# Performance work log

Hardware: AMD Instinct MI355X
Metric: run time of the kernel (lower is better)

The kernel has to match this reference:

```python
import jax, jax.numpy as jnp
from jax import lax
import numpy as np

EPS = 1e-5


def _conv3x3(x, W, stride):
    # x: [N,C,H,W], W: [O,I,3,3]
    return lax.conv_general_dilated(
        x, W, window_strides=(stride, stride), padding=((1, 1), (1, 1)),
        dimension_numbers=("NCHW", "OIHW", "NCHW"))


def _bn(x, gamma, beta):
    # training-mode BatchNorm2d: batch statistics over (N,H,W)
    mean = jnp.mean(x, axis=(0, 2, 3), keepdims=True)
    var = jnp.var(x, axis=(0, 2, 3), keepdims=True)
    inv = lax.rsqrt(var + EPS)
    return (x - mean) * inv * gamma[None, :, None, None] + beta[None, :, None, None]


def setup_inputs() -> dict:
    key = jax.random.key(0)
    ks = jax.random.split(key, 5)
    N, C, H, W = 32, 256, 56, 56
    x = jax.random.normal(ks[0], (N, C, H, W), dtype=jnp.float32)
    W1 = jax.random.normal(ks[1], (C, C, 3, 3), dtype=jnp.float32) * 0.05
    W2 = jax.random.normal(ks[2], (C, C, 3, 3), dtype=jnp.float32) * 0.05
    gamma1 = jnp.ones((C,), jnp.float32)
    beta1 = jnp.zeros((C,), jnp.float32)
    gamma2 = jnp.ones((C,), jnp.float32)
    beta2 = jnp.zeros((C,), jnp.float32)
    mask1 = jax.random.randint(ks[3], (C,), 0, 2).astype(jnp.float32)
    mask2 = jax.random.randint(ks[4], (C,), 0, 2).astype(jnp.float32)
    return {"x": x, "W1": W1, "W2": W2, "gamma1": gamma1, "beta1": beta1,
            "gamma2": gamma2, "beta2": beta2, "mask1": mask1, "mask2": mask2}


def reference(x, W1, W2, gamma1, beta1, gamma2, beta2, mask1, mask2):
    # conv_with_mask: output channels with mask==0 stay zero (structured pruning)
    h = _conv3x3(x, W1, 1) * mask1[None, :, None, None]
    h = jax.nn.relu(_bn(h, gamma1, beta1))
    h = _conv3x3(h, W2, 1) * mask2[None, :, None, None]
    h = _bn(h, gamma2, beta2)
    # stride=1, in_planes==planes -> identity shortcut
    return jax.nn.relu(h + x)
```

## Files before the change

kernel.cpp:

```cpp
#include <hip/hip_runtime.h>

#define N_   32
#define C_   256
#define H_   56
#define W_   56
#define HW_  (H_ * W_)
#define NHW_ (N_ * HW_)
#define PLANE_ ((size_t)NHW_ * 32)

typedef unsigned short u16;
typedef __attribute__((ext_vector_type(8))) short short8;
typedef __attribute__((ext_vector_type(4))) float f32x4;

__device__ __forceinline__ float b2f(u16 u) {
    union { unsigned int i; float f; } v; v.i = ((unsigned int)u) << 16; return v.f;
}
__device__ __forceinline__ u16 f2b(float f) {
    union { float f; unsigned int i; } v; v.f = f;
    unsigned int r = v.i + 0x7fffu + ((v.i >> 16) & 1u);
    return (u16)(r >> 16);
}

typedef const __attribute__((address_space(1))) unsigned int* as1_u32p;
typedef __attribute__((address_space(3))) unsigned int* as3_u32p;
__device__ __forceinline__ void gload_lds16(const u16* g, u16* l) {
    __builtin_amdgcn_global_load_lds((as1_u32p)g, (as3_u32p)l, 16, 0, 0);
}

extern "C" __global__ __launch_bounds__(256) void cvt_x_kernel(
    const float* __restrict__ x, u16* __restrict__ xb)
{
    __shared__ float t[64 * 57];
    const int nh = blockIdx.x, n = nh / H_, h = nh % H_;
    const size_t pix0 = (size_t)(n * H_ + h) * W_;
    for (int cb = 0; cb < 4; ++cb) {
        __syncthreads();
        for (int idx = threadIdx.x; idx < 64 * 56; idx += 256) {
            int cc = idx / 56, w = idx % 56;
            t[cc * 57 + w] = x[(((size_t)(n * C_ + cb * 64 + cc)) * H_ + h) * W_ + w];
        }
        __syncthreads();
        for (int idx = threadIdx.x; idx < 56 * 64; idx += 256) {
            int w = idx >> 6, cc = idx & 63;
            int plane = cb * 2 + (cc >> 5);
            xb[(size_t)plane * PLANE_ + (pix0 + w) * 32 + (cc & 31)] = f2b(t[cc * 57 + w]);
        }
    }
}

extern "C" __global__ void mask_scan_kernel(
    const float* __restrict__ m1, const float* __restrict__ m2,
    int* __restrict__ p1, int* __restrict__ p2,
    float* __restrict__ mp1, float* __restrict__ mp2,
    int* __restrict__ k1, int* __restrict__ k2, int* __restrict__ id256)
{
    const float* mask  = blockIdx.x ? m2 : m1;
    int*   perm  = blockIdx.x ? p2 : p1;
    float* maskp = blockIdx.x ? mp2 : mp1;
    int*   kpar  = blockIdx.x ? k2 : k1;
    __shared__ float m[256];
    const int c = threadIdx.x;
    m[c] = mask[c];
    if (blockIdx.x == 0) id256[c] = c;
    __syncthreads();
    int pre = 0, tot = 0;
    for (int i = 0; i < 256; ++i) {
        int nz = (m[i] != 0.f) ? 1 : 0;
        if (i < c) pre += nz;
        tot += nz;
    }
    const int nz = (m[c] != 0.f) ? 1 : 0;
    const int pos = nz ? pre : tot + (c - pre);
    perm[pos] = c;
    maskp[pos] = m[c];
    if (c == 0) {
        kpar[0] = ((tot + 15) >> 4) << 4;
        kpar[1] = 8;
        kpar[2] = tot;
        kpar[3] = 0;
    }
    if (c < 8) kpar[4 + c] = c;
}

extern "C" __global__ void chunk_sel_kernel(
    const float* __restrict__ shift, const int* __restrict__ kparK,
    int* __restrict__ kpar)
{
    __shared__ int act[8];
    const int c = threadIdx.x;
    if (c < 8) act[c] = 0;
    __syncthreads();
    const int K = kparK[2];
    const bool a = (c < K) || (shift[c] > 0.f);
    if (a) atomicOr(&act[c >> 5], 1);
    __syncthreads();
    if (c == 0) {
        int nq = 0;
        for (int q = 0; q < 8; ++q) if (act[q]) kpar[4 + nq++] = q;
        kpar[1] = nq;
    }
}

extern "C" __global__ __launch_bounds__(256) void pack_w_kernel(
    const float* __restrict__ w, const int* __restrict__ operm,
    const int* __restrict__ iperm, u16* __restrict__ wp)
{
    int o = blockIdx.x * 256 + threadIdx.x;
    int j = o & 7, lq = (o >> 3) & 3, l15 = (o >> 5) & 15;
    int cog = (o >> 9) & 15, cih = (o >> 13) & 7, rs = o >> 16;
    int co = operm[cog * 16 + l15];
    int ci = iperm[cih * 32 + lq * 8 + j];
    wp[o] = f2b(w[((size_t)co * C_ + ci) * 9 + rs]);
}

extern "C" __global__ __launch_bounds__(256, 3) void BasicBlock_4355096838467_kernel(
    const u16* __restrict__ xb,
    const u16* __restrict__ wpA,
    const float* __restrict__ maskp,
    const u16* __restrict__ zeropad,
    const int* __restrict__ kp,
    u16* __restrict__ outb)
{
    __shared__ u16 lds[3][7680];

    const int tid  = threadIdx.x;
    const int wave = tid >> 6, lane = tid & 63;
    const int l15  = lane & 15, lq = lane >> 4;
    const int wave_co = wave >> 1, wave_px = wave & 1;
    const int xcd = blockIdx.x & 7, r_ = blockIdx.x >> 3;
    const int yco = r_ & 1;

    const int Kc = kp[0];
    if (Kc <= yco * 128) return;
    const int nq = kp[1];

    const int sb  = xcd * 112 + (r_ >> 1);
    const int n = sb / 28, hb = sb % 28;
    const int h0 = hb * 2;
    const int cog_base = yco * 8 + wave_co * 4;
    const size_t abase0 = (size_t)cog_base * 512 + (size_t)(l15 * 32 + lq * 8);

    int nf = (Kc >> 4) - cog_base;
    nf = nf < 0 ? 0 : (nf > 4 ? 4 : nf);

    f32x4 acc[4][4];
#pragma unroll
    for (int i = 0; i < 4; ++i)
#pragma unroll
        for (int j = 0; j < 4; ++j) acc[i][j] = (f32x4){0.f, 0.f, 0.f, 0.f};

    auto stage = [&](int q, int b) {
        const u16* plane = xb + (size_t)q * PLANE_;
        for (int is = wave; is < 15; is += 4) {
            int L = is * 64 + lane;
            int pixel = L >> 2, so = L & 3;
            int rr = pixel / 58, slot = pixel - rr * 58;
            int oct = so ^ ((slot >> 1) & 3);
            int row = h0 - 1 + rr, col = slot - 1;
            bool ok = pixel < 232 &&
                      (unsigned)row < (unsigned)H_ && (unsigned)col < (unsigned)W_;
            const u16* gp = ok
                ? plane + ((size_t)(n * H_ + row) * W_ + col) * 32 + oct * 8
                : zeropad + oct * 8;
            gload_lds16(gp, &lds[b][is * 512]);
        }
    };

    short8 afq[3][4];
    auto loadA = [&](int rs_, int q, short8 dst[4]) {
        const size_t bb = (size_t)rs_ * 65536 + (size_t)q * 8192 + abase0;
#pragma unroll
        for (int fm = 0; fm < 4; ++fm)
            if (fm < nf) dst[fm] = *(const short8*)(wpA + bb + (size_t)fm * 512);
    };

    if (nq > 0) {
        const int q0 = kp[4];
        stage(q0, 0);
        __builtin_amdgcn_sched_barrier(0);
        loadA(0, q0, afq[0]);
        loadA(1, q0, afq[1]);
        __builtin_amdgcn_sched_barrier(0);
        if (nq > 1) {
            stage(kp[5], 1);
            __builtin_amdgcn_sched_barrier(0);
            asm volatile("s_waitcnt vmcnt(3)" ::: "memory");
        } else {
            asm volatile("s_waitcnt vmcnt(0)" ::: "memory");
        }
        __builtin_amdgcn_sched_barrier(0);
        __builtin_amdgcn_s_barrier();
        __builtin_amdgcn_sched_barrier(0);

        for (int t = 0; t < nq; ++t) {
            const int q  = kp[4 + t];
            const int qn = kp[4 + (t + 1 < nq ? t + 1 : t)];
            const u16* Lb = &lds[t % 3][0];
            if (nf > 0) {
#pragma unroll
                for (int rs = 0; rs < 9; ++rs) {
                    if (rs < 7) loadA(rs + 2, q, afq[(rs + 2) % 3]);
                    else        loadA(rs - 7, qn, afq[(rs + 2) % 3]);
                    const int r = rs / 3, s = rs - (rs / 3) * 3;
                    short8 bf[4];
#pragma unroll
                    for (int fn = 0; fn < 4; ++fn) {
                        int slot = fn * 16 + l15 + s;
                        int pixel = (wave_px + r) * 58 + slot;
                        int so = lq ^ ((slot >> 1) & 3);
                        bf[fn] = *(const short8*)(Lb + pixel * 32 + so * 8);
                    }
                    __builtin_amdgcn_s_setprio(1);
#pragma unroll
                    for (int fm = 0; fm < 4; ++fm)
                        if (fm < nf) {
#pragma unroll
                            for (int fn = 0; fn < 4; ++fn)
                                acc[fm][fn] = __builtin_amdgcn_mfma_f32_16x16x32_bf16(
                                    afq[rs % 3][fm], bf[fn], acc[fm][fn], 0, 0, 0);
                        }
                    __builtin_amdgcn_s_setprio(0);
                }
            }
            __builtin_amdgcn_sched_barrier(0);
            if (t + 2 < nq) stage(kp[6 + t], (t + 2) % 3);
            __builtin_amdgcn_sched_barrier(0);
            if (t + 1 < nq) {
                if (t + 2 < nq) asm volatile("s_waitcnt vmcnt(3)" ::: "memory");
                else            asm volatile("s_waitcnt vmcnt(0)" ::: "memory");
                __builtin_amdgcn_sched_barrier(0);
                __builtin_amdgcn_s_barrier();
                __builtin_amdgcn_sched_barrier(0);
            }
        }
    }

    const int row = h0 + wave_px;
#pragma unroll
    for (int fn = 0; fn < 4; ++fn) {
        int px = fn * 16 + l15;
        if (px < W_) {
#pragma unroll
            for (int fm = 0; fm < 4; ++fm) {
                int co_b = cog_base * 16 + fm * 16 + lq * 4;
                const f32x4 mk = *(const f32x4*)(maskp + co_b);
                size_t base = (size_t)(co_b >> 5) * PLANE_
                            + ((size_t)(n * H_ + row) * W_ + px) * 32 + (co_b & 31);
                ushort4 o;
                o.x = f2b(acc[fm][fn][0] * mk[0]);
                o.y = f2b(acc[fm][fn][1] * mk[1]);
                o.z = f2b(acc[fm][fn][2] * mk[2]);
                o.w = f2b(acc[fm][fn][3] * mk[3]);
                *(ushort4*)(outb + base) = o;
            }
        }
    }
}

extern "C" __global__ void zero_accum_kernel(float* __restrict__ p) {
    p[blockIdx.x * 256 + threadIdx.x] = 0.f;
}

extern "C" __global__ __launch_bounds__(256) void stats_nhwc_kernel(
    const u16* __restrict__ hb, const int* __restrict__ kp,
    float* __restrict__ gsum, float* __restrict__ gsq)
{
    __shared__ float s_s[8 * 256];
    __shared__ float s_q[8 * 256];
    const int g = threadIdx.x >> 5, l = threadIdx.x & 31;
    const size_t pbase_off = (size_t)(l >> 2) * PLANE_ + (l & 3) * 8;
    const bool live = kp[2] > 128 * (l >> 4);
    float s[8], q[8];
#pragma unroll
    for (int j = 0; j < 8; ++j) { s[j] = 0.f; q[j] = 0.f; }
    const int pbase = blockIdx.x * 256;
    if (live) {
        for (int t = 0; t < 32; ++t) {
            int p = pbase + g + t * 8;
            short8 v = *(const short8*)(hb + pbase_off + (size_t)p * 32);
#pragma unroll
            for (int j = 0; j < 8; ++j) {
                float f = b2f((u16)v[j]);
                s[j] += f; q[j] += f * f;
            }
        }
    }
#pragma unroll
    for (int j = 0; j < 8; ++j) {
        s_s[g * 256 + l * 8 + j] = s[j];
        s_q[g * 256 + l * 8 + j] = q[j];
    }
    __syncthreads();
    const int c = threadIdx.x;
    float S = 0.f, Q = 0.f;
#pragma unroll
    for (int g2 = 0; g2 < 8; ++g2) { S += s_s[g2 * 256 + c]; Q += s_q[g2 * 256 + c]; }
    atomicAdd(&gsum[c], S);
    atomicAdd(&gsq[c], Q);
}

extern "C" __global__ void finalize_bn_kernel(
    const float* __restrict__ gsum, const float* __restrict__ gsq,
    const float* __restrict__ gamma, const float* __restrict__ beta,
    const int* __restrict__ perm,
    float* __restrict__ scale, float* __restrict__ shift)
{
    const int c = threadIdx.x;
    const int co = perm[c];
    const float inv_n = 1.f / (float)NHW_;
    float mean = gsum[c] * inv_n;
    float var  = gsq[c] * inv_n - mean * mean;
    var = fmaxf(var, 0.f);
    float inv = rsqrtf(var + 1e-5f);
    float sc = gamma[co] * inv;
    scale[c] = sc;
    shift[c] = beta[co] - mean * sc;
}

extern "C" __global__ __launch_bounds__(256) void bn_relu_nhwc_kernel(
    u16* __restrict__ hb, const float* __restrict__ scale,
    const float* __restrict__ shift, const int* __restrict__ kp)
{
    size_t idx = ((size_t)blockIdx.x * 256 + threadIdx.x) * 8;
    const int plane = (int)(blockIdx.x / 1568);
    const int c0 = plane * 32 + (int)(idx & 31);
    short8 o;
    if (kp[2] > 128 * (plane >> 2)) {
        short8 v = *(short8*)(hb + idx);
#pragma unroll
        for (int j = 0; j < 8; ++j) {
            float f = b2f((u16)v[j]) * scale[c0 + j] + shift[c0 + j];
            o[j] = (short)f2b(fmaxf(f, 0.f));
        }
    } else {
#pragma unroll
        for (int j = 0; j < 8; ++j)
            o[j] = (short)f2b(fmaxf(shift[c0 + j], 0.f));
    }
    *(short8*)(hb + idx) = o;
}

extern "C" __global__ __launch_bounds__(256) void bn_add_relu_out_kernel(
    const u16* __restrict__ h2b, const float* __restrict__ x,
    const float* __restrict__ scale, const float* __restrict__ shift,
    const int* __restrict__ perm, const int* __restrict__ kp,
    float* __restrict__ out)
{
    __shared__ float t[64 * 57];
    const int nh = blockIdx.x, n = nh / H_, h = nh % H_;
    const size_t pix0 = (size_t)(n * H_ + h) * W_;
    const int K2 = kp[2];
    for (int cb = 0; cb < 4; ++cb) {
        __syncthreads();
        for (int it = threadIdx.x; it < 448; it += 256) {
            int w = it >> 3, oc = it & 7;
            int plane = cb * 2 + (oc >> 2);
            short8 v = {0, 0, 0, 0, 0, 0, 0, 0};
            if (K2 > 128 * (plane >> 2)) {
                size_t addr = (size_t)plane * PLANE_ + (pix0 + w) * 32 + (oc & 3) * 8;
                v = *(const short8*)(h2b + addr);
            }
#pragma unroll
            for (int j = 0; j < 8; ++j) t[(oc * 8 + j) * 57 + w] = b2f((u16)v[j]);
        }
        __syncthreads();
        for (int it = threadIdx.x; it < 64 * 56; it += 256) {
            int cl = it / 56, w = it % 56;
            int c = cb * 64 + cl;
            int co = perm[c];
            size_t oidx = ((size_t)(n * C_ + co) * H_ + h) * W_ + w;
            float v = t[cl * 57 + w] * scale[c] + shift[c] + x[oidx];
            out[oidx] = fmaxf(v, 0.f);
        }
    }
}

extern "C" void kernel_launch(void* const* d_in, const int* in_sizes, int n_in,
                              void* d_out, int out_size, void* d_ws, size_t ws_size,
                              hipStream_t stream) {
    const float* x      = (const float*)d_in[0];
    const float* W1     = (const float*)d_in[1];
    const float* W2     = (const float*)d_in[2];
    const float* gamma1 = (const float*)d_in[3];
    const float* beta1  = (const float*)d_in[4];
    const float* gamma2 = (const float*)d_in[5];
    const float* beta2  = (const float*)d_in[6];
    const float* mask1  = (const float*)d_in[7];
    const float* mask2  = (const float*)d_in[8];
    float* out = (float*)d_out;

    char* ws = (char*)d_ws;
    float* gsum1  = (float*)ws;
    float* gsq1   = gsum1 + 256;
    float* gsum2  = gsq1 + 256;
    float* gsq2   = gsum2 + 256;
    float* scale1 = gsq2 + 256;
    float* shift1 = scale1 + 256;
    float* scale2 = shift1 + 256;
    float* shift2 = scale2 + 256;
    u16*   zeropad = (u16*)(ws + 8192);
    int*   perm1  = (int*)(ws + 12288);
    int*   perm2  = (int*)(ws + 13312);
    float* maskp1 = (float*)(ws + 14336);
    float* maskp2 = (float*)(ws + 15360);
    int*   id256  = (int*)(ws + 16384);
    int*   kpar1  = (int*)(ws + 17408);
    int*   kpar2  = (int*)(ws + 17472);
    u16* Wp1 = (u16*)(ws + 20480);
    u16* Wp2 = Wp1 + 9 * 256 * 256;
    u16* xb  = Wp2 + 9 * 256 * 256;
    u16* h2b = xb;
    u16* h1b = (u16*)d_out;

    zero_accum_kernel<<<dim3(12), dim3(256), 0, stream>>>(gsum1);
    mask_scan_kernel<<<dim3(2), dim3(256), 0, stream>>>(
        mask1, mask2, perm1, perm2, maskp1, maskp2, kpar1, kpar2, id256);
    cvt_x_kernel<<<dim3(N_ * H_), dim3(256), 0, stream>>>(x, xb);
    pack_w_kernel<<<dim3(2304), dim3(256), 0, stream>>>(W1, perm1, id256, Wp1);
    pack_w_kernel<<<dim3(2304), dim3(256), 0, stream>>>(W2, perm2, perm1, Wp2);

    dim3 cgrid(N_ * 56);
    BasicBlock_4355096838467_kernel<<<cgrid, dim3(256), 0, stream>>>(
        xb, Wp1, maskp1, zeropad, kpar1, h1b);
    stats_nhwc_kernel<<<dim3(392), dim3(256), 0, stream>>>(h1b, kpar1, gsum1, gsq1);
    finalize_bn_kernel<<<dim3(1), dim3(256), 0, stream>>>(
        gsum1, gsq1, gamma1, beta1, perm1, scale1, shift1);
    chunk_sel_kernel<<<dim3(1), dim3(256), 0, stream>>>(shift1, kpar1, kpar2);
    bn_relu_nhwc_kernel<<<dim3(12544), dim3(256), 0, stream>>>(h1b, scale1, shift1, kpar1);

    BasicBlock_4355096838467_kernel<<<cgrid, dim3(256), 0, stream>>>(
        h1b, Wp2, maskp2, zeropad, kpar2, h2b);
    stats_nhwc_kernel<<<dim3(392), dim3(256), 0, stream>>>(h2b, kpar2, gsum2, gsq2);
    finalize_bn_kernel<<<dim3(1), dim3(256), 0, stream>>>(
        gsum2, gsq2, gamma2, beta2, perm2, scale2, shift2);
    bn_add_relu_out_kernel<<<dim3(N_ * H_), dim3(256), 0, stream>>>(
        h2b, x, scale2, shift2, perm2, kpar2, out);
}
```

Measured before the change: 590.1 us.

## Fuse BN statistics into conv epilogue and simplify pipeline to double buffering

The conv kernel now reduces per-channel sum and sum-of-squares in its epilogue with wave shuffles and global atomics, which removes the separate stats kernel that re-read the bf16 output. Chunk selection moves into finalize_bn, and bn_relu skips writing planes that the second conv will never read. The main loop drops from three LDS buffers with manual waitcnt, sched_barrier and setprio control to two buffers with __syncthreads. That loses some prefetch depth and the hand-tuned scheduling in exchange for less LDS use. Statistics are now summed from fp32 values before bf16 rounding, and the atomics add contention at the end of each block.

```diff
diff --git a/kernel.cpp b/kernel.cpp
--- a/kernel.cpp
+++ b/kernel.cpp
@@ -77,28 +77,9 @@
         kpar[0] = ((tot + 15) >> 4) << 4;
         kpar[1] = 8;
         kpar[2] = tot;
-        kpar[3] = 0;
+        kpar[3] = 0xff;
     }
     if (c < 8) kpar[4 + c] = c;
-}
-
-extern "C" __global__ void chunk_sel_kernel(
-    const float* __restrict__ shift, const int* __restrict__ kparK,
-    int* __restrict__ kpar)
-{
-    __shared__ int act[8];
-    const int c = threadIdx.x;
-    if (c < 8) act[c] = 0;
-    __syncthreads();
-    const int K = kparK[2];
-    const bool a = (c < K) || (shift[c] > 0.f);
-    if (a) atomicOr(&act[c >> 5], 1);
-    __syncthreads();
-    if (c == 0) {
-        int nq = 0;
-        for (int q = 0; q < 8; ++q) if (act[q]) kpar[4 + nq++] = q;
-        kpar[1] = nq;
-    }
 }
 
 extern "C" __global__ __launch_bounds__(256) void pack_w_kernel(
@@ -119,9 +100,10 @@
     const float* __restrict__ maskp,
     const u16* __restrict__ zeropad,
     const int* __restrict__ kp,
-    u16* __restrict__ outb)
-{
-    __shared__ u16 lds[3][7680];
+    u16* __restrict__ outb,
+    float* __restrict__ gsum, float* __restrict__ gsq)
+{
+    __shared__ u16 lds[2][7680];
 
     const int tid  = threadIdx.x;
     const int wave = tid >> 6, lane = tid & 63;
@@ -177,135 +159,96 @@
     if (nq > 0) {
         const int q0 = kp[4];
         stage(q0, 0);
-        __builtin_amdgcn_sched_barrier(0);
+        __syncthreads();
         loadA(0, q0, afq[0]);
         loadA(1, q0, afq[1]);
-        __builtin_amdgcn_sched_barrier(0);
-        if (nq > 1) {
-            stage(kp[5], 1);
-            __builtin_amdgcn_sched_barrier(0);
-            asm volatile("s_waitcnt vmcnt(3)" ::: "memory");
-        } else {
-            asm volatile("s_waitcnt vmcnt(0)" ::: "memory");
-        }
-        __builtin_amdgcn_sched_barrier(0);
-        __builtin_amdgcn_s_barrier();
-        __builtin_amdgcn_sched_barrier(0);
 
         for (int t = 0; t < nq; ++t) {
             const int q  = kp[4 + t];
             const int qn = kp[4 + (t + 1 < nq ? t + 1 : t)];
-            const u16* Lb = &lds[t % 3][0];
-            if (nf > 0) {
-#pragma unroll
-                for (int rs = 0; rs < 9; ++rs) {
-                    if (rs < 7) loadA(rs + 2, q, afq[(rs + 2) % 3]);
-                    else        loadA(rs - 7, qn, afq[(rs + 2) % 3]);
-                    const int r = rs / 3, s = rs - (rs / 3) * 3;
-                    short8 bf[4];
-#pragma unroll
-                    for (int fn = 0; fn < 4; ++fn) {
-                        int slot = fn * 16 + l15 + s;
-                        int pixel = (wave_px + r) * 58 + slot;
-                        int so = lq ^ ((slot >> 1) & 3);
-                        bf[fn] = *(const short8*)(Lb + pixel * 32 + so * 8);
+            const u16* Lb = &lds[t & 1][0];
+            if (t + 1 < nq) stage(qn, (t + 1) & 1);
+#pragma unroll
+            for (int rs = 0; rs < 9; ++rs) {
+                if (rs < 7) loadA(rs + 2, q, afq[(rs + 2) % 3]);
+                else        loadA(rs - 7, qn, afq[(rs + 2) % 3]);
+                const int r = rs / 3, s = rs - (rs / 3) * 3;
+                short8 bf[4];
+#pragma unroll
+                for (int fn = 0; fn < 4; ++fn) {
+                    int slot = fn * 16 + l15 + s;
+                    int pixel = (wave_px + r) * 58 + slot;
+                    int so = lq ^ ((slot >> 1) & 3);
+                    bf[fn] = *(const short8*)(Lb + pixel * 32 + so * 8);
+                }
+#pragma unroll
+                for (int fm = 0; fm < 4; ++fm)
+                    if (fm < nf) {
+#pragma unroll
+                        for (int fn = 0; fn < 4; ++fn)
+                            acc[fm][fn] = __builtin_amdgcn_mfma_f32_16x16x32_bf16(
+                                afq[rs % 3][fm], bf[fn], acc[fm][fn], 0, 0, 0);
                     }
-                    __builtin_amdgcn_s_setprio(1);
-#pragma unroll
-                    for (int fm = 0; fm < 4; ++fm)
-                        if (fm < nf) {
-#pragma unroll
-                            for (int fn = 0; fn < 4; ++fn)
-                                acc[fm][fn] = __builtin_amdgcn_mfma_f32_16x16x32_bf16(
-                                    afq[rs % 3][fm], bf[fn], acc[fm][fn], 0, 0, 0);
-                        }
-                    __builtin_amdgcn_s_setprio(0);
-                }
             }
-            __builtin_amdgcn_sched_barrier(0);
-            if (t + 2 < nq) stage(kp[6 + t], (t + 2) % 3);
-            __builtin_amdgcn_sched_barrier(0);
-            if (t + 1 < nq) {
-                if (t + 2 < nq) asm volatile("s_waitcnt vmcnt(3)" ::: "memory");
-                else            asm volatile("s_waitcnt vmcnt(0)" ::: "memory");
-                __builtin_amdgcn_sched_barrier(0);
-                __builtin_amdgcn_s_barrier();
-                __builtin_amdgcn_sched_barrier(0);
-            }
+            if (t + 1 < nq) __syncthreads();
         }
     }
 
     const int row = h0 + wave_px;
 #pragma unroll
-    for (int fn = 0; fn < 4; ++fn) {
-        int px = fn * 16 + l15;
-        if (px < W_) {
-#pragma unroll
-            for (int fm = 0; fm < 4; ++fm) {
-                int co_b = cog_base * 16 + fm * 16 + lq * 4;
-                const f32x4 mk = *(const f32x4*)(maskp + co_b);
+    for (int fm = 0; fm < 4; ++fm) {
+        const int co_b = cog_base * 16 + fm * 16 + lq * 4;
+        const f32x4 mk = *(const f32x4*)(maskp + co_b);
+        float s0 = 0.f, s1 = 0.f, s2 = 0.f, s3 = 0.f;
+        float q0 = 0.f, q1 = 0.f, q2 = 0.f, q3 = 0.f;
+#pragma unroll
+        for (int fn = 0; fn < 4; ++fn) {
+            const int px = fn * 16 + l15;
+            if (px < W_) {
+                float v0 = acc[fm][fn][0] * mk[0];
+                float v1 = acc[fm][fn][1] * mk[1];
+                float v2 = acc[fm][fn][2] * mk[2];
+                float v3 = acc[fm][fn][3] * mk[3];
                 size_t base = (size_t)(co_b >> 5) * PLANE_
                             + ((size_t)(n * H_ + row) * W_ + px) * 32 + (co_b & 31);
                 ushort4 o;
-                o.x = f2b(acc[fm][fn][0] * mk[0]);
-                o.y = f2b(acc[fm][fn][1] * mk[1]);
-                o.z = f2b(acc[fm][fn][2] * mk[2]);
-                o.w = f2b(acc[fm][fn][3] * mk[3]);
+                o.x = f2b(v0); o.y = f2b(v1); o.z = f2b(v2); o.w = f2b(v3);
                 *(ushort4*)(outb + base) = o;
+                s0 += v0; s1 += v1; s2 += v2; s3 += v3;
+                q0 += v0 * v0; q1 += v1 * v1; q2 += v2 * v2; q3 += v3 * v3;
             }
+        }
+#pragma unroll
+        for (int off = 1; off < 16; off <<= 1) {
+            s0 += __shfl_xor(s0, off); s1 += __shfl_xor(s1, off);
+            s2 += __shfl_xor(s2, off); s3 += __shfl_xor(s3, off);
+            q0 += __shfl_xor(q0, off); q1 += __shfl_xor(q1, off);
+            q2 += __shfl_xor(q2, off); q3 += __shfl_xor(q3, off);
+        }
+        if (l15 == 0) {
+            atomicAdd(&gsum[co_b + 0], s0); atomicAdd(&gsum[co_b + 1], s1);
+            atomicAdd(&gsum[co_b + 2], s2); atomicAdd(&gsum[co_b + 3], s3);
+            atomicAdd(&gsq[co_b + 0], q0);  atomicAdd(&gsq[co_b + 1], q1);
+            atomicAdd(&gsq[co_b + 2], q2);  atomicAdd(&gsq[co_b + 3], q3);
         }
     }
 }
 
 extern "C" __global__ void zero_accum_kernel(float* __restrict__ p) {
     p[blockIdx.x * 256 + threadIdx.x] = 0.f;
-}
-
-extern "C" __global__ __launch_bounds__(256) void stats_nhwc_kernel(
-    const u16* __restrict__ hb, const int* __restrict__ kp,
-    float* __restrict__ gsum, float* __restrict__ gsq)
-{
-    __shared__ float s_s[8 * 256];
-    __shared__ float s_q[8 * 256];
-    const int g = threadIdx.x >> 5, l = threadIdx.x & 31;
-    const size_t pbase_off = (size_t)(l >> 2) * PLANE_ + (l & 3) * 8;
-    const bool live = kp[2] > 128 * (l >> 4);
-    float s[8], q[8];
-#pragma unroll
-    for (int j = 0; j < 8; ++j) { s[j] = 0.f; q[j] = 0.f; }
-    const int pbase = blockIdx.x * 256;
-    if (live) {
-        for (int t = 0; t < 32; ++t) {
-            int p = pbase + g + t * 8;
-            short8 v = *(const short8*)(hb + pbase_off + (size_t)p * 32);
-#pragma unroll
-            for (int j = 0; j < 8; ++j) {
-                float f = b2f((u16)v[j]);
-                s[j] += f; q[j] += f * f;
-            }
-        }
-    }
-#pragma unroll
-    for (int j = 0; j < 8; ++j) {
-        s_s[g * 256 + l * 8 + j] = s[j];
-        s_q[g * 256 + l * 8 + j] = q[j];
-    }
-    __syncthreads();
-    const int c = threadIdx.x;
-    float S = 0.f, Q = 0.f;
-#pragma unroll
-    for (int g2 = 0; g2 < 8; ++g2) { S += s_s[g2 * 256 + c]; Q += s_q[g2 * 256 + c]; }
-    atomicAdd(&gsum[c], S);
-    atomicAdd(&gsq[c], Q);
 }
 
 extern "C" __global__ void finalize_bn_kernel(
     const float* __restrict__ gsum, const float* __restrict__ gsq,
     const float* __restrict__ gamma, const float* __restrict__ beta,
-    const int* __restrict__ perm,
-    float* __restrict__ scale, float* __restrict__ shift)
-{
+    const int* __restrict__ perm, const int* __restrict__ kparK,
+    float* __restrict__ scale, float* __restrict__ shift,
+    int* __restrict__ kparOut)
+{
+    __shared__ float sh[256];
+    __shared__ int actm;
     const int c = threadIdx.x;
+    if (c == 0) actm = 0;
     const int co = perm[c];
     const float inv_n = 1.f / (float)NHW_;
     float mean = gsum[c] * inv_n;
@@ -313,19 +256,34 @@
     var = fmaxf(var, 0.f);
     float inv = rsqrtf(var + 1e-5f);
     float sc = gamma[co] * inv;
+    float shv = beta[co] - mean * sc;
     scale[c] = sc;
-    shift[c] = beta[co] - mean * sc;
+    shift[c] = shv;
+    sh[c] = shv;
+    __syncthreads();
+    if (kparOut) {
+        const int K = kparK[2];
+        if (c < K || sh[c] > 0.f) atomicOr(&actm, 1 << (c >> 5));
+        __syncthreads();
+        if (c == 0) {
+            int m = actm, nq = 0;
+            for (int qq = 0; qq < 8; ++qq) if ((m >> qq) & 1) kparOut[4 + nq++] = qq;
+            kparOut[1] = nq;
+            kparOut[3] = m;
+        }
+    }
 }
 
 extern "C" __global__ __launch_bounds__(256) void bn_relu_nhwc_kernel(
     u16* __restrict__ hb, const float* __restrict__ scale,
-    const float* __restrict__ shift, const int* __restrict__ kp)
+    const float* __restrict__ shift, const int* __restrict__ kpK,
+    const int* __restrict__ kpQ)
 {
     size_t idx = ((size_t)blockIdx.x * 256 + threadIdx.x) * 8;
     const int plane = (int)(blockIdx.x / 1568);
     const int c0 = plane * 32 + (int)(idx & 31);
     short8 o;
-    if (kp[2] > 128 * (plane >> 2)) {
+    if (kpK[2] > 128 * (plane >> 2)) {
         short8 v = *(short8*)(hb + idx);
 #pragma unroll
         for (int j = 0; j < 8; ++j) {
@@ -333,6 +291,7 @@
             o[j] = (short)f2b(fmaxf(f, 0.f));
         }
     } else {
+        if (!((kpQ[3] >> plane) & 1)) return;
 #pragma unroll
         for (int j = 0; j < 8; ++j)
             o[j] = (short)f2b(fmaxf(shift[c0 + j], 0.f));
@@ -421,18 +380,16 @@
 
     dim3 cgrid(N_ * 56);
     BasicBlock_4355096838467_kernel<<<cgrid, dim3(256), 0, stream>>>(
-        xb, Wp1, maskp1, zeropad, kpar1, h1b);
-    stats_nhwc_kernel<<<dim3(392), dim3(256), 0, stream>>>(h1b, kpar1, gsum1, gsq1);
+        xb, Wp1, maskp1, zeropad, kpar1, h1b, gsum1, gsq1);
     finalize_bn_kernel<<<dim3(1), dim3(256), 0, stream>>>(
-        gsum1, gsq1, gamma1, beta1, perm1, scale1, shift1);
-    chunk_sel_kernel<<<dim3(1), dim3(256), 0, stream>>>(shift1, kpar1, kpar2);
-    bn_relu_nhwc_kernel<<<dim3(12544), dim3(256), 0, stream>>>(h1b, scale1, shift1, kpar1);
+        gsum1, gsq1, gamma1, beta1, perm1, kpar1, scale1, shift1, kpar2);
+    bn_relu_nhwc_kernel<<<dim3(12544), dim3(256), 0, stream>>>(
+        h1b, scale1, shift1, kpar1, kpar2);
 
     BasicBlock_4355096838467_kernel<<<cgrid, dim3(256), 0, stream>>>(
-        h1b, Wp2, maskp2, zeropad, kpar2, h2b);
-    stats_nhwc_kernel<<<dim3(392), dim3(256), 0, stream>>>(h2b, kpar2, gsum2, gsq2);
+        h1b, Wp2, maskp2, zeropad, kpar2, h2b, gsum2, gsq2);
     finalize_bn_kernel<<<dim3(1), dim3(256), 0, stream>>>(
-        gsum2, gsq2, gamma2, beta2, perm2, scale2, shift2);
+        gsum2, gsq2, gamma2, beta2, perm2, kpar2, scale2, shift2, (int*)nullptr);
     bn_add_relu_out_kernel<<<dim3(N_ * H_), dim3(256), 0, stream>>>(
         h2b, x, scale2, shift2, perm2, kpar2, out);
 }
```

After: 802.4 us. +36.0%, slower.
